# Performance work log

Measured on AMD Instinct MI355X. Metric: run time of the kernel, lower is better.

Reference implementation:

```python
import jax, jax.numpy as jnp
import numpy as np

NHEAD = 8
HB, WB = 16, 16  # block_size


def _mha(q, k, v, w_in, b_in, w_out, b_out, nhead):
    # q,k,v: [L, B, C] seq-first, like torch.nn.MultiheadAttention (eval mode, no dropout)
    Lq, B, C = q.shape
    d = C // nhead
    wq, wk, wv = jnp.split(w_in, 3, axis=0)
    bq, bk, bv = jnp.split(b_in, 3)
    qh = (q @ wq.T + bq).reshape(Lq, B, nhead, d).transpose(1, 2, 0, 3)        # [B,H,Lq,d]
    kh = (k @ wk.T + bk).reshape(k.shape[0], B, nhead, d).transpose(1, 2, 0, 3)
    vh = (v @ wv.T + bv).reshape(v.shape[0], B, nhead, d).transpose(1, 2, 0, 3)
    scale = 1.0 / jnp.sqrt(jnp.asarray(d, dtype=qh.dtype))
    scores = jnp.einsum('bhqd,bhkd->bhqk', qh * scale, kh)
    attn = jax.nn.softmax(scores, axis=-1)
    out = jnp.einsum('bhqk,bhkd->bhqd', attn, vh)                               # [B,H,Lq,d]
    out = out.transpose(2, 0, 1, 3).reshape(Lq, B, C)
    return out @ w_out.T + b_out


def setup_inputs() -> dict:
    key = jax.random.key(0)
    ks = jax.random.split(key, 12)
    n, c, t, h, w = 2, 256, 2, 64, 64
    q = jax.random.normal(ks[0], (n, c, t, h, w), dtype=jnp.float32)
    k = jax.random.normal(ks[1], (n, c, t, h, w), dtype=jnp.float32)
    v = jax.random.normal(ks[2], (n, c, t, h, w), dtype=jnp.float32)
    pos = jax.random.normal(ks[3], (n, c, t, h, w), dtype=jnp.float32)
    s = 0.02
    wl_in = jax.random.normal(ks[4], (3 * c, c), dtype=jnp.float32) * s
    bl_in = jnp.zeros((3 * c,), dtype=jnp.float32)
    wl_out = jax.random.normal(ks[5], (c, c), dtype=jnp.float32) * s
    bl_out = jnp.zeros((c,), dtype=jnp.float32)
    ws_in = jax.random.normal(ks[6], (3 * c, c), dtype=jnp.float32) * s
    bs_in = jnp.zeros((3 * c,), dtype=jnp.float32)
    ws_out = jax.random.normal(ks[7], (c, c), dtype=jnp.float32) * s
    bs_out = jnp.zeros((c,), dtype=jnp.float32)
    return {"q": q, "k": k, "v": v, "pos": pos,
            "wl_in": wl_in, "bl_in": bl_in, "wl_out": wl_out, "bl_out": bl_out,
            "ws_in": ws_in, "bs_in": bs_in, "ws_out": ws_out, "bs_out": bs_out}


def reference(q, k, v, pos, wl_in, bl_in, wl_out, bl_out, ws_in, bs_in, ws_out, bs_out):
    n, c, t_q, h, w = q.shape
    t_k = k.shape[2]
    bn_h, bn_w = h // HB, w // WB

    def to_long(x, t):
        # [n,c,t,h,w] -> [t*bn_h*bn_w, n*HB*WB, c]
        x = x.reshape(n, c, t, bn_h, HB, bn_w, WB).transpose(2, 3, 5, 0, 4, 6, 1)
        return x.reshape(t * bn_h * bn_w, n * HB * WB, c)

    ql = to_long(q, t_q)
    kl = to_long(k, t_k)
    vl = to_long(v, t_k)
    pl = to_long(pos, t_q)

    v1 = _mha(ql + pl, kl + pl, vl, wl_in, bl_in, wl_out, bl_out, NHEAD)

    def long_to_short(x):
        # [t*bn_h*bn_w, n*HB*WB, c] -> [t*HB*WB, n*bn_h*bn_w, c]
        x = x.reshape(t_q, bn_h, bn_w, n, HB, WB, c).transpose(0, 4, 5, 3, 1, 2, 6)
        return x.reshape(t_q * HB * WB, n * bn_h * bn_w, c)

    v2 = long_to_short(v1)
    ps = long_to_short(pl)

    out = _mha(v2 + ps, v2 + ps, v2, ws_in, bs_in, ws_out, bs_out, NHEAD)
    out = out.reshape(t_q, HB, WB, n, bn_h, bn_w, c).transpose(3, 6, 0, 4, 1, 5, 2)
    return out.reshape(n, c, t_q, h, w)
```

## Files before the change

kernel.cpp:

```cpp
#include <hip/hip_runtime.h>
#include <math.h>


#define SCALE_D32 0.17677669529663687f
#define EXP2_SCALE 0.25508680987930193f
#define GLOBAL_AS __attribute__((address_space(1)))
#define LDS_AS __attribute__((address_space(3)))

typedef short short8 __attribute__((ext_vector_type(8)));
typedef short short4v __attribute__((ext_vector_type(4)));
typedef short short2v __attribute__((ext_vector_type(2)));
typedef float floatx4 __attribute__((ext_vector_type(4)));

__device__ __forceinline__ short f2bf(float f) {
  union { float f; unsigned u; } x;
  x.f = f;
  unsigned r = x.u + 0x7fffu + ((x.u >> 16) & 1u);
  return (short)(r >> 16);
}
__device__ __forceinline__ float bf2f(short s) {
  union { unsigned u; float f; } x;
  x.u = ((unsigned)(unsigned short)s) << 16;
  return x.f;
}

__device__ __forceinline__ int o1s_phys(int q, int ch) {
  return q * 256 + (ch & ~63) + ((((ch >> 3) & 7) ^ (q & 7)) << 3) + (ch & 7);
}

__device__ __forceinline__ void stage_w(short* Wsl, const short* Wg, int kb,
                                        int wave, int lane, int rsub, int csub) {
#pragma unroll
  for (int j = 0; j < 8; ++j) {
    int r0 = (wave * 8 + j) * 8;
    int row = r0 + rsub;
    int c = csub ^ (row & 7);
    const short* gp = Wg + (long)row * 256 + kb * 64 + c * 8;
    short* lp = &Wsl[r0 * 64 + lane * 8];
    __builtin_amdgcn_global_load_lds((const GLOBAL_AS void*)gp,
                                     (LDS_AS void*)lp, 16, 0, 0);
  }
}

__global__ __launch_bounds__(256) void pack_kernel(
    const float* __restrict__ q, const float* __restrict__ k,
    const float* __restrict__ v, const float* __restrict__ pos,
    short* __restrict__ Xp, short* __restrict__ Xq,
    short* __restrict__ Xk, short* __restrict__ Xv,
    const float* __restrict__ wl_in, const float* __restrict__ wl_out,
    const float* __restrict__ ws_in, const float* __restrict__ ws_out,
    short* __restrict__ wbf) {
  __shared__ float tP[64][65];
  __shared__ float tX[64][65];
  int b = blockIdx.x;
  int cb = b & 3;
  int h  = (b >> 2) & 63;
  int nt = b >> 8;
  int n = nt >> 1, t = nt & 1;
  int c0 = cb * 64;
  int bh = h >> 4, ii = h & 15;
  long inbase = (long)n * 2097152 + (long)t * 4096 + (long)h * 64;
  int tx = threadIdx.x & 63;
  int ty = threadIdx.x >> 6;

  for (int cc = ty; cc < 64; cc += 4) {
    long a = inbase + (long)(c0 + cc) * 8192 + tx;
    tP[cc][tx] = pos[a];
    tX[cc][tx] = q[a];
  }
  __syncthreads();
  for (int ww = ty; ww < 64; ww += 4) {
    int bw = ww >> 4, j = ww & 15;
    int m1 = (((t * 4 + bh) * 4 + bw) * 512) + n * 256 + ii * 16 + j;
    long o = (long)m1 * 256 + c0 + tx;
    float pv = tP[tx][ww];
    Xp[o] = f2bf(pv);
    Xq[o] = f2bf(tX[tx][ww] + pv);
  }
  __syncthreads();
  for (int cc = ty; cc < 64; cc += 4) {
    long a = inbase + (long)(c0 + cc) * 8192 + tx;
    tX[cc][tx] = k[a];
  }
  __syncthreads();
  for (int ww = ty; ww < 64; ww += 4) {
    int bw = ww >> 4, j = ww & 15;
    int m1 = (((t * 4 + bh) * 4 + bw) * 512) + n * 256 + ii * 16 + j;
    long o = (long)m1 * 256 + c0 + tx;
    Xk[o] = f2bf(tX[tx][ww] + tP[tx][ww]);
  }
  __syncthreads();
  for (int cc = ty; cc < 64; cc += 4) {
    long a = inbase + (long)(c0 + cc) * 8192 + tx;
    tX[cc][tx] = v[a];
  }
  __syncthreads();
  for (int ww = ty; ww < 64; ww += 4) {
    int bw = ww >> 4, j = ww & 15;
    int m1 = (((t * 4 + bh) * 4 + bw) * 512) + n * 256 + ii * 16 + j;
    long o = (long)m1 * 256 + c0 + tx;
    Xv[o] = f2bf(tX[tx][ww]);
  }
  int idx = (blockIdx.x * 256 + threadIdx.x) * 2;
  const float* wp;
  if (idx < 196608) wp = wl_in + idx;
  else if (idx < 262144) wp = wl_out + (idx - 196608);
  else if (idx < 458752) wp = ws_in + (idx - 262144);
  else wp = ws_out + (idx - 458752);
  float2 wv = *(const float2*)wp;
  wbf[idx] = f2bf(wv.x);
  wbf[idx + 1] = f2bf(wv.y);
}

template <bool OUT32>
__global__ __launch_bounds__(256) void gemm_tri(
    const short* __restrict__ A0, const short* __restrict__ A1,
    const short* __restrict__ A2, const short* __restrict__ W0,
    const float* __restrict__ bias0, void* __restrict__ C0,
    void* __restrict__ C1, void* __restrict__ C2) {
  __shared__ short As[128 * 64];
  __shared__ short Ws[64 * 64];
  int z = blockIdx.z;
  const short* A = (z == 0) ? A0 : ((z == 1) ? A1 : A2);
  const short* Wb = W0 + z * 65536;
  const float* bias = bias0 + z * 256;
  void* Csel = (z == 0) ? C0 : ((z == 1) ? C1 : C2);
  int m0 = blockIdx.x * 128;
  int n0 = blockIdx.y * 64;
  int tid = threadIdx.x;
  int lane = tid & 63, wave = tid >> 6;
  int wm = wave >> 1, wn = wave & 1;
  int l15 = lane & 15, quad = lane >> 4;
  int x7 = l15 & 7;
  int rsub = lane >> 3;
  int csub = lane & 7;

  floatx4 acc[4][2];
#pragma unroll
  for (int mt = 0; mt < 4; ++mt)
#pragma unroll
    for (int nt = 0; nt < 2; ++nt) acc[mt][nt] = (floatx4)(0.f);

  for (int kb = 0; kb < 4; ++kb) {
    int k0 = kb * 64;
    if (kb) __syncthreads();
#pragma unroll
    for (int j = 0; j < 4; ++j) {
      int r0 = (wave * 4 + j) * 8;
      int row = r0 + rsub;
      int c = csub ^ (row & 7);
      const short* gp = A + (long)(m0 + row) * 256 + k0 + c * 8;
      short* lp = &As[r0 * 64 + lane * 8];
      __builtin_amdgcn_global_load_lds((const GLOBAL_AS void*)gp,
                                       (LDS_AS void*)lp, 16, 0, 0);
    }
#pragma unroll
    for (int j = 0; j < 2; ++j) {
      int r0 = (wave * 2 + j) * 8;
      int row = r0 + rsub;
      int c = csub ^ (row & 7);
      const short* gp = Wb + (long)(n0 + row) * 256 + k0 + c * 8;
      short* lp = &Ws[r0 * 64 + lane * 8];
      __builtin_amdgcn_global_load_lds((const GLOBAL_AS void*)gp,
                                       (LDS_AS void*)lp, 16, 0, 0);
    }
    __syncthreads();
#pragma unroll
    for (int ks = 0; ks < 2; ++ks) {
      int pc = (ks * 4 + quad) ^ x7;
      short8 af[4], bfr[2];
#pragma unroll
      for (int mt = 0; mt < 4; ++mt) {
        int row = wm * 64 + mt * 16 + l15;
        af[mt] = *(const short8*)&As[row * 64 + pc * 8];
      }
#pragma unroll
      for (int nt = 0; nt < 2; ++nt) {
        int row = wn * 32 + nt * 16 + l15;
        bfr[nt] = *(const short8*)&Ws[row * 64 + pc * 8];
      }
#pragma unroll
      for (int mt = 0; mt < 4; ++mt)
#pragma unroll
        for (int nt = 0; nt < 2; ++nt)
          acc[mt][nt] = __builtin_amdgcn_mfma_f32_16x16x32_bf16(
              af[mt], bfr[nt], acc[mt][nt], 0, 0, 0);
    }
  }
  float bia0 = bias[n0 + wn * 32 + l15];
  float bia1 = bias[n0 + wn * 32 + 16 + l15];
#pragma unroll
  for (int mt = 0; mt < 4; ++mt) {
#pragma unroll
    for (int r = 0; r < 4; ++r) {
      int row = m0 + wm * 64 + mt * 16 + quad * 4 + r;
      long base = (long)row * 256 + n0 + wn * 32 + l15;
      if (OUT32) {
        float* C = (float*)Csel;
        C[base] = acc[mt][0][r] + bia0;
        C[base + 16] = acc[mt][1][r] + bia1;
      } else {
        short* C = (short*)Csel;
        C[base] = f2bf(acc[mt][0][r] + bia0);
        C[base + 16] = f2bf(acc[mt][1][r] + bia1);
      }
    }
  }
}

__global__ __launch_bounds__(256) void attn1_mega(
    const short* __restrict__ Q1, const short* __restrict__ K1,
    const short* __restrict__ V1, const short* __restrict__ Xp,
    const short* __restrict__ Wo, const float* __restrict__ bias_o,
    const short* __restrict__ Wsin, const float* __restrict__ bias_sin,
    short* __restrict__ Q2, short* __restrict__ K2, short* __restrict__ V2) {
  __shared__ union {
    struct {
      short Vs[32][264];
      short Vt[4][32][40];
      short Pw[4][32][40];
    } a;
    struct {
      short O1s[32 * 256];
      short Vins[32 * 256];
      short Ws[256 * 64];
    } g;
  } u;
  int b1 = blockIdx.x;
  int tid = threadIdx.x;
  int wave = tid >> 6, lane = tid & 63;
  int l15 = lane & 15, quad = lane >> 4;
  int x7 = l15 & 7;
  int rsub = lane >> 3;
  int csub = lane & 7;

#pragma unroll
  for (int p = 0; p < 4; ++p) {
    int idx = p * 256 + tid;
    int row = idx >> 5;
    int c8 = idx & 31;
    *(short8*)&u.a.Vs[row][c8 * 8] =
        *(const short8*)(V1 + ((long)row * 512 + b1) * 256 + c8 * 8);
  }
  __syncthreads();

  int key = lane & 31;
  int dh = (lane >> 5) * 16;
  int pc2 = 2 * (key & 15) + (key >> 4);

  floatx4 oacc[2][4];
  float lsum[2][2][4];

#pragma unroll
  for (int h2 = 0; h2 < 2; ++h2) {
    int hh = wave * 2 + h2;
    long fbase = ((long)l15 * 512 + b1) * 256 + hh * 32 + quad * 8;
    short8 qf0 = *(const short8*)(Q1 + fbase);
    short8 qf1 = *(const short8*)(Q1 + fbase + 16 * 512 * 256);
    short8 kf0 = *(const short8*)(K1 + fbase);
    short8 kf1 = *(const short8*)(K1 + fbase + 16 * 512 * 256);
    short8 v0 = *(const short8*)&u.a.Vs[key][hh * 32 + dh];
    short8 v1 = *(const short8*)&u.a.Vs[key][hh * 32 + dh + 8];
#pragma unroll
    for (int j = 0; j < 8; ++j) {
      u.a.Vt[wave][dh + j][pc2] = v0[j];
      u.a.Vt[wave][dh + 8 + j][pc2] = v1[j];
    }
    floatx4 s00 = __builtin_amdgcn_mfma_f32_16x16x32_bf16(qf0, kf0, (floatx4)(0.f), 0, 0, 0);
    floatx4 s01 = __builtin_amdgcn_mfma_f32_16x16x32_bf16(qf0, kf1, (floatx4)(0.f), 0, 0, 0);
    floatx4 s10 = __builtin_amdgcn_mfma_f32_16x16x32_bf16(qf1, kf0, (floatx4)(0.f), 0, 0, 0);
    floatx4 s11 = __builtin_amdgcn_mfma_f32_16x16x32_bf16(qf1, kf1, (floatx4)(0.f), 0, 0, 0);
    float li0[4], li1[4];
#pragma unroll
    for (int r = 0; r < 4; ++r) {
      float p00 = __builtin_amdgcn_exp2f(s00[r] * EXP2_SCALE);
      float p01 = __builtin_amdgcn_exp2f(s01[r] * EXP2_SCALE);
      float p10 = __builtin_amdgcn_exp2f(s10[r] * EXP2_SCALE);
      float p11 = __builtin_amdgcn_exp2f(s11[r] * EXP2_SCALE);
      li0[r] = p00 + p01;
      li1[r] = p10 + p11;
      short2v pa, pb;
      pa.x = f2bf(p00); pa.y = f2bf(p01);
      pb.x = f2bf(p10); pb.y = f2bf(p11);
      *(short2v*)&u.a.Pw[wave][quad * 4 + r][2 * l15] = pa;
      *(short2v*)&u.a.Pw[wave][16 + quad * 4 + r][2 * l15] = pb;
    }
#pragma unroll
    for (int r = 0; r < 4; ++r) {
      li0[r] += __shfl_xor(li0[r], 1, 64);
      li0[r] += __shfl_xor(li0[r], 2, 64);
      li0[r] += __shfl_xor(li0[r], 4, 64);
      li0[r] += __shfl_xor(li0[r], 8, 64);
      li1[r] += __shfl_xor(li1[r], 1, 64);
      li1[r] += __shfl_xor(li1[r], 2, 64);
      li1[r] += __shfl_xor(li1[r], 4, 64);
      li1[r] += __shfl_xor(li1[r], 8, 64);
      lsum[h2][0][r] = li0[r];
      lsum[h2][1][r] = li1[r];
    }
    short8 pf0 = *(const short8*)&u.a.Pw[wave][l15][quad * 8];
    short8 pf1 = *(const short8*)&u.a.Pw[wave][16 + l15][quad * 8];
    short8 vt0 = *(const short8*)&u.a.Vt[wave][l15][quad * 8];
    short8 vt1 = *(const short8*)&u.a.Vt[wave][16 + l15][quad * 8];
    oacc[h2][0] = __builtin_amdgcn_mfma_f32_16x16x32_bf16(pf0, vt0, (floatx4)(0.f), 0, 0, 0);
    oacc[h2][1] = __builtin_amdgcn_mfma_f32_16x16x32_bf16(pf0, vt1, (floatx4)(0.f), 0, 0, 0);
    oacc[h2][2] = __builtin_amdgcn_mfma_f32_16x16x32_bf16(pf1, vt0, (floatx4)(0.f), 0, 0, 0);
    oacc[h2][3] = __builtin_amdgcn_mfma_f32_16x16x32_bf16(pf1, vt1, (floatx4)(0.f), 0, 0, 0);
  }

  __syncthreads();

#pragma unroll
  for (int h2 = 0; h2 < 2; ++h2) {
    int hh = wave * 2 + h2;
    int cA = hh * 32 + l15;
    int cB = cA + 16;
#pragma unroll
    for (int r = 0; r < 4; ++r) {
      float inv0 = 1.f / lsum[h2][0][r];
      float inv1 = 1.f / lsum[h2][1][r];
      int qa = quad * 4 + r, qb = 16 + quad * 4 + r;
      u.g.O1s[o1s_phys(qa, cA)] = f2bf(oacc[h2][0][r] * inv0);
      u.g.O1s[o1s_phys(qa, cB)] = f2bf(oacc[h2][1][r] * inv0);
      u.g.O1s[o1s_phys(qb, cA)] = f2bf(oacc[h2][2][r] * inv1);
      u.g.O1s[o1s_phys(qb, cB)] = f2bf(oacc[h2][3][r] * inv1);
    }
  }

  floatx4 acc1[2][4];
#pragma unroll
  for (int mt = 0; mt < 2; ++mt)
#pragma unroll
    for (int nt = 0; nt < 4; ++nt) acc1[mt][nt] = (floatx4)(0.f);

  for (int kb = 0; kb < 4; ++kb) {
    __syncthreads();
    stage_w(u.g.Ws, Wo, kb, wave, lane, rsub, csub);
    __syncthreads();
#pragma unroll
    for (int ks = 0; ks < 2; ++ks) {
      int pc = (ks * 4 + quad) ^ x7;
      short8 af[2], bfr[4];
#pragma unroll
      for (int mt = 0; mt < 2; ++mt)
        af[mt] = *(const short8*)&u.g.O1s[(mt * 16 + l15) * 256 + kb * 64 + pc * 8];
#pragma unroll
      for (int nt = 0; nt < 4; ++nt)
        bfr[nt] = *(const short8*)&u.g.Ws[(wave * 64 + nt * 16 + l15) * 64 + pc * 8];
#pragma unroll
      for (int mt = 0; mt < 2; ++mt)
#pragma unroll
        for (int nt = 0; nt < 4; ++nt)
          acc1[mt][nt] = __builtin_amdgcn_mfma_f32_16x16x32_bf16(
              af[mt], bfr[nt], acc1[mt][nt], 0, 0, 0);
    }
  }

  __syncthreads();
  {
    float bvo[4];
#pragma unroll
    for (int nt = 0; nt < 4; ++nt) bvo[nt] = bias_o[wave * 64 + nt * 16 + l15];
#pragma unroll
    for (int mt = 0; mt < 2; ++mt) {
#pragma unroll
      for (int r = 0; r < 4; ++r) {
        int qrow = mt * 16 + quad * 4 + r;
        long pbase = ((long)qrow * 512 + b1) * 256;
#pragma unroll
        for (int nt = 0; nt < 4; ++nt) {
          int col = wave * 64 + nt * 16 + l15;
          float val = acc1[mt][nt][r] + bvo[nt];
          int ph = o1s_phys(qrow, col);
          u.g.Vins[ph] = f2bf(val);
          u.g.O1s[ph] = f2bf(val + bf2f(Xp[pbase + col]));
        }
      }
    }
  }

  int nn = b1 >> 8, ii = (b1 >> 4) & 15, jj = b1 & 15;
#pragma unroll
  for (int z = 0; z < 3; ++z) {
    const short* Wz = Wsin + z * 65536;
    const short* Ab = (z < 2) ? (const short*)u.g.O1s : (const short*)u.g.Vins;
    short* outz = (z == 0) ? Q2 : ((z == 1) ? K2 : V2);
    float bz[4];
#pragma unroll
    for (int nt = 0; nt < 4; ++nt)
      bz[nt] = bias_sin[z * 256 + wave * 64 + nt * 16 + l15];

    floatx4 acc[2][4];
#pragma unroll
    for (int mt = 0; mt < 2; ++mt)
#pragma unroll
      for (int nt = 0; nt < 4; ++nt) acc[mt][nt] = (floatx4)(0.f);

    for (int kb = 0; kb < 4; ++kb) {
      __syncthreads();
      stage_w(u.g.Ws, Wz, kb, wave, lane, rsub, csub);
      __syncthreads();
#pragma unroll
      for (int ks = 0; ks < 2; ++ks) {
        int pc = (ks * 4 + quad) ^ x7;
        short8 af[2], bfr[4];
#pragma unroll
        for (int mt = 0; mt < 2; ++mt)
          af[mt] = *(const short8*)&Ab[(mt * 16 + l15) * 256 + kb * 64 + pc * 8];
#pragma unroll
        for (int nt = 0; nt < 4; ++nt)
          bfr[nt] = *(const short8*)&u.g.Ws[(wave * 64 + nt * 16 + l15) * 64 + pc * 8];
#pragma unroll
        for (int mt = 0; mt < 2; ++mt)
#pragma unroll
          for (int nt = 0; nt < 4; ++nt)
            acc[mt][nt] = __builtin_amdgcn_mfma_f32_16x16x32_bf16(
                af[mt], bfr[nt], acc[mt][nt], 0, 0, 0);
      }
    }

#pragma unroll
    for (int mt = 0; mt < 2; ++mt) {
#pragma unroll
      for (int r = 0; r < 4; ++r) {
        int qrow = mt * 16 + quad * 4 + r;
        int t = qrow >> 4, bh = (qrow >> 2) & 3, bw = qrow & 3;
        int m2 = (t * 256 + ii * 16 + jj) * 32 + nn * 16 + bh * 4 + bw;
        long xbase = (long)m2 * 256;
#pragma unroll
        for (int nt = 0; nt < 4; ++nt) {
          int col = wave * 64 + nt * 16 + l15;
          outz[xbase + col] = f2bf(acc[mt][nt][r] + bz[nt]);
        }
      }
    }
  }
}

__global__ __launch_bounds__(256) void attn2_mfma(
    const short* __restrict__ Q2, const short* __restrict__ K2,
    const short* __restrict__ V2, short* __restrict__ O2) {
  __shared__ short Ks[64][40];
  __shared__ short Vt[32][72];
  __shared__ short Pw[4][16][72];
  int bid = blockIdx.x;
  int rest = bid & 255;
  int qblk = bid >> 8;
  int hh = 2 * (rest & 3) + (rest >> 7);
  int b2 = (rest >> 2) & 31;
  int tid = threadIdx.x;
  int wave = tid >> 6, lane = tid & 63;
  int l15 = lane & 15, quad = lane >> 4;

  short8 qf;
  {
    long tok = (long)(qblk * 64 + wave * 16 + l15) * 32 + b2;
    qf = *(const short8*)(Q2 + tok * 256 + hh * 32 + quad * 8);
  }
  floatx4 Oa = (floatx4)(0.f), Ob = (floatx4)(0.f);
  float li[4] = {0.f, 0.f, 0.f, 0.f};

  int skey = tid >> 2;
  int sd0 = (tid & 3) * 8;
  int vkey = lane;
  int vd0 = wave * 8;
  int vcol = (vkey & 15) * 4 + (vkey >> 4);

  for (int kb = 0; kb < 8; ++kb) {
    if (kb) __syncthreads();
    {
      long tok = (long)(kb * 64 + skey) * 32 + b2;
      *(short8*)&Ks[skey][sd0] = *(const short8*)(K2 + tok * 256 + hh * 32 + sd0);
    }
    {
      long tok = (long)(kb * 64 + vkey) * 32 + b2;
      short8 v = *(const short8*)(V2 + tok * 256 + hh * 32 + vd0);
#pragma unroll
      for (int j = 0; j < 8; ++j) Vt[vd0 + j][vcol] = v[j];
    }
    __syncthreads();
    floatx4 st[4];
#pragma unroll
    for (int kt = 0; kt < 4; ++kt) {
      short8 kf = *(const short8*)&Ks[kt * 16 + l15][quad * 8];
      st[kt] = __builtin_amdgcn_mfma_f32_16x16x32_bf16(qf, kf, (floatx4)(0.f), 0, 0, 0);
    }
#pragma unroll
    for (int r = 0; r < 4; ++r) {
      float p0 = __builtin_amdgcn_exp2f(st[0][r] * EXP2_SCALE);
      float p1 = __builtin_amdgcn_exp2f(st[1][r] * EXP2_SCALE);
      float p2 = __builtin_amdgcn_exp2f(st[2][r] * EXP2_SCALE);
      float p3 = __builtin_amdgcn_exp2f(st[3][r] * EXP2_SCALE);
      li[r] += (p0 + p1) + (p2 + p3);
      short4v pp;
      pp.x = f2bf(p0); pp.y = f2bf(p1); pp.z = f2bf(p2); pp.w = f2bf(p3);
      *(short4v*)&Pw[wave][quad * 4 + r][l15 * 4] = pp;
    }
#pragma unroll
    for (int kk = 0; kk < 2; ++kk) {
      short8 pf = *(const short8*)&Pw[wave][l15][kk * 32 + quad * 8];
      short8 v0 = *(const short8*)&Vt[l15][kk * 32 + quad * 8];
      short8 v1 = *(const short8*)&Vt[16 + l15][kk * 32 + quad * 8];
      Oa = __builtin_amdgcn_mfma_f32_16x16x32_bf16(pf, v0, Oa, 0, 0, 0);
      Ob = __builtin_amdgcn_mfma_f32_16x16x32_bf16(pf, v1, Ob, 0, 0, 0);
    }
  }
#pragma unroll
  for (int r = 0; r < 4; ++r) {
    float s = li[r];
    s += __shfl_xor(s, 1, 64);
    s += __shfl_xor(s, 2, 64);
    s += __shfl_xor(s, 4, 64);
    s += __shfl_xor(s, 8, 64);
    float inv = 1.f / s;
    long tok = (long)(qblk * 64 + wave * 16 + quad * 4 + r) * 32 + b2;
    long a = tok * 256 + hh * 32 + l15;
    O2[a] = f2bf(Oa[r] * inv);
    O2[a + 16] = f2bf(Ob[r] * inv);
  }
}

__global__ __launch_bounds__(256) void unpack_kernel(
    const float* __restrict__ Y, float* __restrict__ out) {
  __shared__ float tl[64][65];
  int b = blockIdx.x;
  int cb = b & 3;
  int h = (b >> 2) & 63;
  int nt = b >> 8;
  int n = nt >> 1, t = nt & 1;
  int c0 = cb * 64;
  int bh = h >> 4, ii = h & 15;
  int tx = threadIdx.x & 63;
  int ty = threadIdx.x >> 6;
  for (int ww = ty; ww < 64; ww += 4) {
    int bw = ww >> 4, j = ww & 15;
    int l2 = t * 256 + ii * 16 + j;
    int b2 = n * 16 + bh * 4 + bw;
    int m2 = l2 * 32 + b2;
    tl[tx][ww] = Y[(long)m2 * 256 + c0 + tx];
  }
  __syncthreads();
  long ob = (long)n * 2097152 + (long)t * 4096 + (long)h * 64 + tx;
  for (int cc = ty; cc < 64; cc += 4) {
    out[ob + (long)(c0 + cc) * 8192] = tl[cc][tx];
  }
}

extern "C" void kernel_launch(void* const* d_in, const int* in_sizes, int n_in,
                              void* d_out, int out_size, void* d_ws, size_t ws_size,
                              hipStream_t stream) {
  const float* q      = (const float*)d_in[0];
  const float* k      = (const float*)d_in[1];
  const float* v      = (const float*)d_in[2];
  const float* pos    = (const float*)d_in[3];
  const float* wl_in  = (const float*)d_in[4];
  const float* bl_in  = (const float*)d_in[5];
  const float* wl_out = (const float*)d_in[6];
  const float* bl_out = (const float*)d_in[7];
  const float* ws_in  = (const float*)d_in[8];
  const float* bs_in  = (const float*)d_in[9];
  const float* ws_out = (const float*)d_in[10];
  const float* bs_out = (const float*)d_in[11];
  float* out = (float*)d_out;
  char* wsb = (char*)d_ws;
  const size_t SLB = 16777216;
  short* s0 = (short*)(wsb);
  short* wbf = (short*)(wsb + SLB / 2);
  short* s1 = (short*)(wsb + SLB);
  short* s2 = (short*)(wsb + 2 * SLB);
  short* s3 = (short*)(wsb + 3 * SLB);
  short* s4 = (short*)(wsb + 4 * SLB);
  short* s5 = (short*)(wsb + 5 * SLB);
  short* s6 = (short*)(wsb + 6 * SLB);

  pack_kernel<<<1024, 256, 0, stream>>>(q, k, v, pos, s0, s1, s2, s3,
                                        wl_in, wl_out, ws_in, ws_out, wbf);

  dim3 g3(128, 4, 3);
  dim3 g1(128, 4, 1);
  gemm_tri<false><<<g3, 256, 0, stream>>>(s1, s2, s3, wbf, bl_in, s4, s5, s6);

  attn1_mega<<<512, 256, 0, stream>>>(s4, s5, s6, s0, wbf + 196608, bl_out,
                                      wbf + 262144, bs_in, s1, s2, s3);

  attn2_mfma<<<2048, 256, 0, stream>>>(s1, s2, s3, s4);
  gemm_tri<true><<<g1, 256, 0, stream>>>(s4, s4, s4, wbf + 458752, bs_out,
                                         s2, s2, s2);

  unpack_kernel<<<1024, 256, 0, stream>>>((const float*)s2, out);
}
```

Measured before the change: 203.1 us.

## Fuse first-stage QKV input projection into attention mega-kernel

Removes the separate gemm_tri launch for the long-attention Q/K/V input projections and computes them inside the attention kernel. Each block stages its 32-row input tiles into LDS and projects them with the staged weights, leaving the projected Q/K/V in swizzled LDS instead of writing them to global memory and reading them back. This saves a kernel launch and a global round trip of the projected activations. In exchange, LDS use per block grows to about 80KB, which may lower occupancy, and each block serializes three more small GEMMs.

```diff
diff --git a/kernel.cpp b/kernel.cpp
--- a/kernel.cpp
+++ b/kernel.cpp
@@ -37,6 +37,21 @@
     int c = csub ^ (row & 7);
     const short* gp = Wg + (long)row * 256 + kb * 64 + c * 8;
     short* lp = &Wsl[r0 * 64 + lane * 8];
+    __builtin_amdgcn_global_load_lds((const GLOBAL_AS void*)gp,
+                                     (LDS_AS void*)lp, 16, 0, 0);
+  }
+}
+
+__device__ __forceinline__ void stage_tile(short* dst, const short* Xg,
+                                           int b1, int tid) {
+#pragma unroll
+  for (int p = 0; p < 4; ++p) {
+    int idx = p * 256 + tid;
+    int row = idx >> 5;
+    int ch = idx & 31;
+    int chs = (ch & ~7) | ((ch & 7) ^ (row & 7));
+    const short* gp = Xg + ((long)(row * 512 + b1)) * 256 + chs * 8;
+    short* lp = dst + idx * 8;
     __builtin_amdgcn_global_load_lds((const GLOBAL_AS void*)gp,
                                      (LDS_AS void*)lp, 16, 0, 0);
   }
@@ -208,24 +223,17 @@
   }
 }
 
-__global__ __launch_bounds__(256) void attn1_mega(
-    const short* __restrict__ Q1, const short* __restrict__ K1,
-    const short* __restrict__ V1, const short* __restrict__ Xp,
+__global__ __launch_bounds__(256) void attn1_giga(
+    const short* __restrict__ Xq, const short* __restrict__ Xk,
+    const short* __restrict__ Xv, const short* __restrict__ Xp,
+    const short* __restrict__ Wlin, const float* __restrict__ bias_lin,
     const short* __restrict__ Wo, const float* __restrict__ bias_o,
     const short* __restrict__ Wsin, const float* __restrict__ bias_sin,
     short* __restrict__ Q2, short* __restrict__ K2, short* __restrict__ V2) {
-  __shared__ union {
-    struct {
-      short Vs[32][264];
-      short Vt[4][32][40];
-      short Pw[4][32][40];
-    } a;
-    struct {
-      short O1s[32 * 256];
-      short Vins[32 * 256];
-      short Ws[256 * 64];
-    } g;
-  } u;
+  __shared__ short R1[32 * 256];
+  __shared__ short R2[32 * 256];
+  __shared__ short R3[32 * 256];
+  __shared__ short R4[256 * 64];
   int b1 = blockIdx.x;
   int tid = threadIdx.x;
   int wave = tid >> 6, lane = tid & 63;
@@ -234,16 +242,61 @@
   int rsub = lane >> 3;
   int csub = lane & 7;
 
-#pragma unroll
-  for (int p = 0; p < 4; ++p) {
-    int idx = p * 256 + tid;
-    int row = idx >> 5;
-    int c8 = idx & 31;
-    *(short8*)&u.a.Vs[row][c8 * 8] =
-        *(const short8*)(V1 + ((long)row * 512 + b1) * 256 + c8 * 8);
-  }
-  __syncthreads();
-
+  floatx4 acc[2][4];
+
+#pragma unroll 1
+  for (int z = 0; z < 3; ++z) {
+    short* Rz = (z == 0) ? R1 : ((z == 1) ? R2 : R3);
+    const short* Xg = (z == 0) ? Xq : ((z == 1) ? Xk : Xv);
+    const short* Wz = Wlin + z * 65536;
+    stage_tile(Rz, Xg, b1, tid);
+#pragma unroll
+    for (int mt = 0; mt < 2; ++mt)
+#pragma unroll
+      for (int nt = 0; nt < 4; ++nt) acc[mt][nt] = (floatx4)(0.f);
+    for (int kb = 0; kb < 4; ++kb) {
+      __syncthreads();
+      stage_w(R4, Wz, kb, wave, lane, rsub, csub);
+      __syncthreads();
+#pragma unroll
+      for (int ks = 0; ks < 2; ++ks) {
+        int pc = (ks * 4 + quad) ^ x7;
+        short8 af[2], bfr[4];
+#pragma unroll
+        for (int mt = 0; mt < 2; ++mt)
+          af[mt] = *(const short8*)&Rz[(mt * 16 + l15) * 256 + kb * 64 + pc * 8];
+#pragma unroll
+        for (int nt = 0; nt < 4; ++nt)
+          bfr[nt] = *(const short8*)&R4[(wave * 64 + nt * 16 + l15) * 64 + pc * 8];
+#pragma unroll
+        for (int mt = 0; mt < 2; ++mt)
+#pragma unroll
+          for (int nt = 0; nt < 4; ++nt)
+            acc[mt][nt] = __builtin_amdgcn_mfma_f32_16x16x32_bf16(
+                af[mt], bfr[nt], acc[mt][nt], 0, 0, 0);
+      }
+    }
+    __syncthreads();
+    float bz[4];
+#pragma unroll
+    for (int nt = 0; nt < 4; ++nt)
+      bz[nt] = bias_lin[z * 256 + wave * 64 + nt * 16 + l15];
+#pragma unroll
+    for (int mt = 0; mt < 2; ++mt)
+#pragma unroll
+      for (int r = 0; r < 4; ++r) {
+        int row = mt * 16 + quad * 4 + r;
+#pragma unroll
+        for (int nt = 0; nt < 4; ++nt) {
+          int col = wave * 64 + nt * 16 + l15;
+          Rz[o1s_phys(row, col)] = f2bf(acc[mt][nt][r] + bz[nt]);
+        }
+      }
+  }
+  __syncthreads();
+
+  short* Vtb = R4;
+  short* Pwb = R4 + 5120;
   int key = lane & 31;
   int dh = (lane >> 5) * 16;
   int pc2 = 2 * (key & 15) + (key >> 4);
@@ -254,17 +307,17 @@
 #pragma unroll
   for (int h2 = 0; h2 < 2; ++h2) {
     int hh = wave * 2 + h2;
-    long fbase = ((long)l15 * 512 + b1) * 256 + hh * 32 + quad * 8;
-    short8 qf0 = *(const short8*)(Q1 + fbase);
-    short8 qf1 = *(const short8*)(Q1 + fbase + 16 * 512 * 256);
-    short8 kf0 = *(const short8*)(K1 + fbase);
-    short8 kf1 = *(const short8*)(K1 + fbase + 16 * 512 * 256);
-    short8 v0 = *(const short8*)&u.a.Vs[key][hh * 32 + dh];
-    short8 v1 = *(const short8*)&u.a.Vs[key][hh * 32 + dh + 8];
+    int cb0 = hh * 32 + quad * 8;
+    short8 qf0 = *(const short8*)&R1[o1s_phys(l15, cb0)];
+    short8 qf1 = *(const short8*)&R1[o1s_phys(l15 + 16, cb0)];
+    short8 kf0 = *(const short8*)&R2[o1s_phys(l15, cb0)];
+    short8 kf1 = *(const short8*)&R2[o1s_phys(l15 + 16, cb0)];
+    short8 v0 = *(const short8*)&R3[o1s_phys(key, hh * 32 + dh)];
+    short8 v1 = *(const short8*)&R3[o1s_phys(key, hh * 32 + dh + 8)];
 #pragma unroll
     for (int j = 0; j < 8; ++j) {
-      u.a.Vt[wave][dh + j][pc2] = v0[j];
-      u.a.Vt[wave][dh + 8 + j][pc2] = v1[j];
+      Vtb[(wave * 32 + dh + j) * 40 + pc2] = v0[j];
+      Vtb[(wave * 32 + dh + 8 + j) * 40 + pc2] = v1[j];
     }
     floatx4 s00 = __builtin_amdgcn_mfma_f32_16x16x32_bf16(qf0, kf0, (floatx4)(0.f), 0, 0, 0);
     floatx4 s01 = __builtin_amdgcn_mfma_f32_16x16x32_bf16(qf0, kf1, (floatx4)(0.f), 0, 0, 0);
@@ -282,8 +335,8 @@
       short2v pa, pb;
       pa.x = f2bf(p00); pa.y = f2bf(p01);
       pb.x = f2bf(p10); pb.y = f2bf(p11);
-      *(short2v*)&u.a.Pw[wave][quad * 4 + r][2 * l15] = pa;
-      *(short2v*)&u.a.Pw[wave][16 + quad * 4 + r][2 * l15] = pb;
+      *(short2v*)&Pwb[(wave * 32 + quad * 4 + r) * 40 + 2 * l15] = pa;
+      *(short2v*)&Pwb[(wave * 32 + 16 + quad * 4 + r) * 40 + 2 * l15] = pb;
     }
 #pragma unroll
     for (int r = 0; r < 4; ++r) {
@@ -298,10 +351,10 @@
       lsum[h2][0][r] = li0[r];
       lsum[h2][1][r] = li1[r];
     }
-    short8 pf0 = *(const short8*)&u.a.Pw[wave][l15][quad * 8];
-    short8 pf1 = *(const short8*)&u.a.Pw[wave][16 + l15][quad * 8];
-    short8 vt0 = *(const short8*)&u.a.Vt[wave][l15][quad * 8];
-    short8 vt1 = *(const short8*)&u.a.Vt[wave][16 + l15][quad * 8];
+    short8 pf0 = *(const short8*)&Pwb[(wave * 32 + l15) * 40 + quad * 8];
+    short8 pf1 = *(const short8*)&Pwb[(wave * 32 + 16 + l15) * 40 + quad * 8];
+    short8 vt0 = *(const short8*)&Vtb[(wave * 32 + l15) * 40 + quad * 8];
+    short8 vt1 = *(const short8*)&Vtb[(wave * 32 + 16 + l15) * 40 + quad * 8];
     oacc[h2][0] = __builtin_amdgcn_mfma_f32_16x16x32_bf16(pf0, vt0, (floatx4)(0.f), 0, 0, 0);
     oacc[h2][1] = __builtin_amdgcn_mfma_f32_16x16x32_bf16(pf0, vt1, (floatx4)(0.f), 0, 0, 0);
     oacc[h2][2] = __builtin_amdgcn_mfma_f32_16x16x32_bf16(pf1, vt0, (floatx4)(0.f), 0, 0, 0);
@@ -320,22 +373,20 @@
       float inv0 = 1.f / lsum[h2][0][r];
       float inv1 = 1.f / lsum[h2][1][r];
       int qa = quad * 4 + r, qb = 16 + quad * 4 + r;
-      u.g.O1s[o1s_phys(qa, cA)] = f2bf(oacc[h2][0][r] * inv0);
-      u.g.O1s[o1s_phys(qa, cB)] = f2bf(oacc[h2][1][r] * inv0);
-      u.g.O1s[o1s_phys(qb, cA)] = f2bf(oacc[h2][2][r] * inv1);
-      u.g.O1s[o1s_phys(qb, cB)] = f2bf(oacc[h2][3][r] * inv1);
-    }
-  }
-
-  floatx4 acc1[2][4];
+      R1[o1s_phys(qa, cA)] = f2bf(oacc[h2][0][r] * inv0);
+      R1[o1s_phys(qa, cB)] = f2bf(oacc[h2][1][r] * inv0);
+      R1[o1s_phys(qb, cA)] = f2bf(oacc[h2][2][r] * inv1);
+      R1[o1s_phys(qb, cB)] = f2bf(oacc[h2][3][r] * inv1);
+    }
+  }
+
 #pragma unroll
   for (int mt = 0; mt < 2; ++mt)
 #pragma unroll
-    for (int nt = 0; nt < 4; ++nt) acc1[mt][nt] = (floatx4)(0.f);
-
+    for (int nt = 0; nt < 4; ++nt) acc[mt][nt] = (floatx4)(0.f);
   for (int kb = 0; kb < 4; ++kb) {
     __syncthreads();
-    stage_w(u.g.Ws, Wo, kb, wave, lane, rsub, csub);
+    stage_w(R4, Wo, kb, wave, lane, rsub, csub);
     __syncthreads();
 #pragma unroll
     for (int ks = 0; ks < 2; ++ks) {
@@ -343,16 +394,16 @@
       short8 af[2], bfr[4];
 #pragma unroll
       for (int mt = 0; mt < 2; ++mt)
-        af[mt] = *(const short8*)&u.g.O1s[(mt * 16 + l15) * 256 + kb * 64 + pc * 8];
+        af[mt] = *(const short8*)&R1[(mt * 16 + l15) * 256 + kb * 64 + pc * 8];
 #pragma unroll
       for (int nt = 0; nt < 4; ++nt)
-        bfr[nt] = *(const short8*)&u.g.Ws[(wave * 64 + nt * 16 + l15) * 64 + pc * 8];
+        bfr[nt] = *(const short8*)&R4[(wave * 64 + nt * 16 + l15) * 64 + pc * 8];
 #pragma unroll
       for (int mt = 0; mt < 2; ++mt)
 #pragma unroll
         for (int nt = 0; nt < 4; ++nt)
-          acc1[mt][nt] = __builtin_amdgcn_mfma_f32_16x16x32_bf16(
-              af[mt], bfr[nt], acc1[mt][nt], 0, 0, 0);
+          acc[mt][nt] = __builtin_amdgcn_mfma_f32_16x16x32_bf16(
+              af[mt], bfr[nt], acc[mt][nt], 0, 0, 0);
     }
   }
 
@@ -370,35 +421,32 @@
 #pragma unroll
         for (int nt = 0; nt < 4; ++nt) {
           int col = wave * 64 + nt * 16 + l15;
-          float val = acc1[mt][nt][r] + bvo[nt];
+          float val = acc[mt][nt][r] + bvo[nt];
           int ph = o1s_phys(qrow, col);
-          u.g.Vins[ph] = f2bf(val);
-          u.g.O1s[ph] = f2bf(val + bf2f(Xp[pbase + col]));
+          R3[ph] = f2bf(val);
+          R2[ph] = f2bf(val + bf2f(Xp[pbase + col]));
         }
       }
     }
   }
 
   int nn = b1 >> 8, ii = (b1 >> 4) & 15, jj = b1 & 15;
-#pragma unroll
+#pragma unroll 1
   for (int z = 0; z < 3; ++z) {
     const short* Wz = Wsin + z * 65536;
-    const short* Ab = (z < 2) ? (const short*)u.g.O1s : (const short*)u.g.Vins;
+    const short* Ab = (z < 2) ? R2 : R3;
     short* outz = (z == 0) ? Q2 : ((z == 1) ? K2 : V2);
     float bz[4];
 #pragma unroll
     for (int nt = 0; nt < 4; ++nt)
       bz[nt] = bias_sin[z * 256 + wave * 64 + nt * 16 + l15];
-
-    floatx4 acc[2][4];
 #pragma unroll
     for (int mt = 0; mt < 2; ++mt)
 #pragma unroll
       for (int nt = 0; nt < 4; ++nt) acc[mt][nt] = (floatx4)(0.f);
-
     for (int kb = 0; kb < 4; ++kb) {
       __syncthreads();
-      stage_w(u.g.Ws, Wz, kb, wave, lane, rsub, csub);
+      stage_w(R4, Wz, kb, wave, lane, rsub, csub);
       __syncthreads();
 #pragma unroll
       for (int ks = 0; ks < 2; ++ks) {
@@ -409,7 +457,7 @@
           af[mt] = *(const short8*)&Ab[(mt * 16 + l15) * 256 + kb * 64 + pc * 8];
 #pragma unroll
         for (int nt = 0; nt < 4; ++nt)
-          bfr[nt] = *(const short8*)&u.g.Ws[(wave * 64 + nt * 16 + l15) * 64 + pc * 8];
+          bfr[nt] = *(const short8*)&R4[(wave * 64 + nt * 16 + l15) * 64 + pc * 8];
 #pragma unroll
         for (int mt = 0; mt < 2; ++mt)
 #pragma unroll
@@ -418,7 +466,6 @@
                 af[mt], bfr[nt], acc[mt][nt], 0, 0, 0);
       }
     }
-
 #pragma unroll
     for (int mt = 0; mt < 2; ++mt) {
 #pragma unroll
@@ -576,15 +623,13 @@
   pack_kernel<<<1024, 256, 0, stream>>>(q, k, v, pos, s0, s1, s2, s3,
                                         wl_in, wl_out, ws_in, ws_out, wbf);
 
-  dim3 g3(128, 4, 3);
+  attn1_giga<<<512, 256, 0, stream>>>(s1, s2, s3, s0, wbf, bl_in,
+                                      wbf + 196608, bl_out,
+                                      wbf + 262144, bs_in, s4, s5, s6);
+
+  attn2_mfma<<<2048, 256, 0, stream>>>(s4, s5, s6, s1);
   dim3 g1(128, 4, 1);
-  gemm_tri<false><<<g3, 256, 0, stream>>>(s1, s2, s3, wbf, bl_in, s4, s5, s6);
-
-  attn1_mega<<<512, 256, 0, stream>>>(s4, s5, s6, s0, wbf + 196608, bl_out,
-                                      wbf + 262144, bs_in, s1, s2, s3);
-
-  attn2_mfma<<<2048, 256, 0, stream>>>(s1, s2, s3, s4);
-  gemm_tri<true><<<g1, 256, 0, stream>>>(s4, s4, s4, wbf + 458752, bs_out,
+  gemm_tri<true><<<g1, 256, 0, stream>>>(s1, s1, s1, wbf + 458752, bs_out,
                                          s2, s2, s2);
 
   unpack_kernel<<<1024, 256, 0, stream>>>((const float*)s2, out);
```

Result: no change. 202.8 us (-0.2%).
